# Performance work log

Measured on AMD Instinct MI355X. Metric: run time of the kernel, lower is better.

## Reference

```python
import jax, jax.numpy as jnp
import numpy as np
import math

B, N, T, D, H, NOUT = 32, 20, 100, 4, 128, 16
E = N * (N - 1)
EPS = 1e-5

def _conv1d(x, w, b):
    # x: [M, Cin, L], w: [Cout, Cin, K] -> [M, Cout, L-K+1] (VALID, stride 1)
    y = jax.lax.conv_general_dilated(x, w, (1,), 'VALID', dimension_numbers=('NCH', 'OIH', 'NCH'))
    return y + b[None, :, None]

def _bn(x, g, b, axes, caxis):
    # training-mode batch norm (biased variance), eps as in torch
    m = jnp.mean(x, axis=axes, keepdims=True)
    v = jnp.var(x, axis=axes, keepdims=True)
    sh = [1] * x.ndim
    sh[caxis] = -1
    return (x - m) / jnp.sqrt(v + EPS) * g.reshape(sh) + b.reshape(sh)

def _mlp(x, w1, b1, w2, b2, g, bb):
    h = jax.nn.elu(x @ w1.T + b1)
    h = jax.nn.elu(h @ w2.T + b2)
    return _bn(h, g, bb, (0, 1), 2)  # BN over B*E samples per feature

def _forward(rel_rec, rel_send, inputs, conv1_w, conv1_b, bn1_g, bn1_b, conv2_w, conv2_b, bn2_g, bn2_b, pred_w, pred_b, att_w, att_b, mlp1_w1, mlp1_b1, mlp1_w2, mlp1_b2, mlp1_g, mlp1_bb, mlp2_w1, mlp2_b1, mlp2_w2, mlp2_b2, mlp2_g, mlp2_bb, mlp3_w1, mlp3_b1, mlp3_w2, mlp3_b2, mlp3_g, mlp3_bb, fc_out_w, fc_out_b):
    Bv, Nv, Tv, Dv = inputs.shape
    Ev = Nv * (Nv - 1)
    # node2edge_temporal: gather sender/receiver trajectories -> [B*E, 2D, T]
    xf = inputs.reshape(Bv, Nv, Tv * Dv)
    recv = jnp.einsum('en,bnf->bef', rel_rec, xf).reshape(Bv * Ev, Tv, Dv).transpose(0, 2, 1)
    send = jnp.einsum('en,bnf->bef', rel_send, xf).reshape(Bv * Ev, Tv, Dv).transpose(0, 2, 1)
    edges = jnp.concatenate([send, recv], axis=1)
    # CNN over time
    h = jax.nn.relu(_conv1d(edges, conv1_w, conv1_b))
    h = _bn(h, bn1_g, bn1_b, (0, 2), 1)
    L = h.shape[-1] // 2
    h = h[:, :, : 2 * L].reshape(h.shape[0], h.shape[1], L, 2).max(axis=-1)  # maxpool k=2 s=2
    h = jax.nn.relu(_conv1d(h, conv2_w, conv2_b))
    h = _bn(h, bn2_g, bn2_b, (0, 2), 1)
    pred = jnp.einsum('bct,oc->bot', h, pred_w[:, :, 0]) + pred_b[None, :, None]
    att = jax.nn.softmax(jnp.einsum('bct,oc->bot', h, att_w[:, :, 0]) + att_b[None, :, None], axis=-1)
    x = (pred * att).mean(axis=-1).reshape(Bv, Ev, -1)  # attention-weighted mean pool
    x = _mlp(x, mlp1_w1, mlp1_b1, mlp1_w2, mlp1_b2, mlp1_g, mlp1_bb)
    x_skip = x
    # edge2node: scatter-mean into receivers (divide by N)
    xn = jnp.einsum('en,beh->bnh', rel_rec, x) / Nv
    xn = _mlp(xn, mlp2_w1, mlp2_b1, mlp2_w2, mlp2_b2, mlp2_g, mlp2_bb)
    # node2edge: gather back to edges
    es = jnp.einsum('en,bnh->beh', rel_send, xn)
    er = jnp.einsum('en,bnh->beh', rel_rec, xn)
    x = jnp.concatenate([es, er, x_skip], axis=2)
    x = _mlp(x, mlp3_w1, mlp3_b1, mlp3_w2, mlp3_b2, mlp3_g, mlp3_bb)
    return x @ fc_out_w.T + fc_out_b

def setup_inputs() -> dict:
    key = jax.random.key(0)
    ks = iter(jax.random.split(key, 64))
    def rn(shape, scale):
        return jax.random.normal(next(ks), shape, dtype=jnp.float32) * scale
    def xav(fo, fi):
        return rn((fo, fi), math.sqrt(2.0 / (fo + fi)))
    inputs = rn((B, N, T, D), 1.0)
    pairs = np.array([(i, j) for i in range(N) for j in range(N) if i != j])
    eye = np.eye(N, dtype=np.float32)
    d = {'inputs': inputs,
         'rel_rec': jnp.asarray(eye[pairs[:, 0]]),
         'rel_send': jnp.asarray(eye[pairs[:, 1]])}
    d['conv1_w'] = rn((H, 2 * D, 5), math.sqrt(2.0 / (5 * H)))
    d['conv1_b'] = jnp.full((H,), 0.1, jnp.float32)
    d['bn1_g'] = jnp.ones((H,), jnp.float32); d['bn1_b'] = jnp.zeros((H,), jnp.float32)
    d['conv2_w'] = rn((H, H, 5), math.sqrt(2.0 / (5 * H)))
    d['conv2_b'] = jnp.full((H,), 0.1, jnp.float32)
    d['bn2_g'] = jnp.ones((H,), jnp.float32); d['bn2_b'] = jnp.zeros((H,), jnp.float32)
    d['pred_w'] = rn((H, H, 1), math.sqrt(2.0 / H))
    d['pred_b'] = jnp.full((H,), 0.1, jnp.float32)
    d['att_w'] = rn((1, H, 1), math.sqrt(2.0))
    d['att_b'] = jnp.full((1,), 0.1, jnp.float32)
    for nm, fi in (('mlp1', H), ('mlp2', H), ('mlp3', 3 * H)):
        d[nm + '_w1'] = xav(H, fi); d[nm + '_b1'] = jnp.full((H,), 0.1, jnp.float32)
        d[nm + '_w2'] = xav(H, H); d[nm + '_b2'] = jnp.full((H,), 0.1, jnp.float32)
        d[nm + '_g'] = jnp.ones((H,), jnp.float32); d[nm + '_bb'] = jnp.zeros((H,), jnp.float32)
    d['fc_out_w'] = xav(NOUT, H)
    d['fc_out_b'] = jnp.full((NOUT,), 0.1, jnp.float32)
    return d

def reference(inputs, rel_rec, rel_send, conv1_w, conv1_b, bn1_g, bn1_b, conv2_w, conv2_b, bn2_g, bn2_b, pred_w, pred_b, att_w, att_b, mlp1_w1, mlp1_b1, mlp1_w2, mlp1_b2, mlp1_g, mlp1_bb, mlp2_w1, mlp2_b1, mlp2_w2, mlp2_b2, mlp2_g, mlp2_bb, mlp3_w1, mlp3_b1, mlp3_w2, mlp3_b2, mlp3_g, mlp3_bb, fc_out_w, fc_out_b):
    return _forward(rel_rec, rel_send, inputs, conv1_w, conv1_b, bn1_g, bn1_b, conv2_w, conv2_b, bn2_g, bn2_b, pred_w, pred_b, att_w, att_b, mlp1_w1, mlp1_b1, mlp1_w2, mlp1_b2, mlp1_g, mlp1_bb, mlp2_w1, mlp2_b1, mlp2_w2, mlp2_b2, mlp2_g, mlp2_bb, mlp3_w1, mlp3_b1, mlp3_w2, mlp3_b2, mlp3_g, mlp3_bb, fc_out_w, fc_out_b)
```

## Files before the change

kernel.cpp:

```cpp
#include <hip/hip_runtime.h>
#include <hip/hip_bf16.h>
#include <hip/hip_fp16.h>

#define BB 32
#define NN 20
#define TT 100
#define DD 4
#define HH 128
#define EE 380
#define BE 12160
#define L1 96
#define LP 48
#define L2 44
#define NOUT 16
#define EPS 1e-5f
#define NREP 64

typedef _Float16 f16x8 __attribute__((ext_vector_type(8)));
typedef _Float16 f16x4 __attribute__((ext_vector_type(4)));
typedef _Float16 f16x2 __attribute__((ext_vector_type(2)));
typedef float f32x4 __attribute__((ext_vector_type(4)));

#define S_BN1_SC 256
#define S_BN2_SC 768
#define S_M1_SC 1280
#define S_M2_SC 1792
#define S_M3_SC 2304

#define OFF_STATS 0ULL
#define OFF_SIDX 16384ULL
#define OFF_RIDX 18432ULL
#define OFF_INC 20480ULL
#define OFF_Y23 24576ULL
#define OFF_X 149446656ULL
#define OFF_BUFA 155672576ULL
#define OFF_BUFB 161898496ULL
#define OFF_XN 168124416ULL
#define OFF_T640 168452096ULL
#define OFF_REPM 168779776ULL
#define OFF_HF16 168845312ULL
#define OFF_MP 171958272ULL
#define OFF_APACK OFF_T640
#define OFF_APACK1 (OFF_T640 + 163840ULL)
#define OFF_PWT (OFF_T640 + 180224ULL)
#define OFF_REP1 OFF_BUFA
#define OFF_REP2 (OFF_BUFA + 65536ULL)
#define MP_M1W1 0
#define MP_M1W2 16384
#define MP_M2W1 32768
#define MP_M2W2 49152
#define MP_M3W2 65536
#define MP_M3W1 81920

__device__ __forceinline__ float eluf(float v) { return v > 0.f ? v : expm1f(v); }

__global__ __launch_bounds__(256) void k_prep(const float* __restrict__ rel_rec,
                                              const float* __restrict__ rel_send,
                                              const float* __restrict__ w2,
                                              const float* __restrict__ w1,
                                              const float* __restrict__ pred_w,
                                              const float* __restrict__ m1w1,
                                              const float* __restrict__ m1w2,
                                              const float* __restrict__ m2w1,
                                              const float* __restrict__ m2w2,
                                              const float* __restrict__ m3w1,
                                              const float* __restrict__ m3w2,
                                              _Float16* __restrict__ apack,
                                              _Float16* __restrict__ apack1,
                                              float* __restrict__ pwt,
                                              _Float16* __restrict__ mp,
                                              float* rep1, float* rep2, float* repm,
                                              int* sidx, int* ridx, int* inc) {
    int b = blockIdx.x;
    int tid = threadIdx.x;
    int l = tid & 63;
    if (b < 40) {
        int f = b * 4 + (tid >> 6);
        int m0 = f & 7, ks = f >> 3, s = ks & 3, k = ks >> 2;
        int m = m0 * 16 + (l & 15);
        int cbase = 32 * s + (l >> 4) * 8;
#pragma unroll
        for (int j = 0; j < 8; ++j)
            apack[(f * 64 + l) * 8 + j] = (_Float16)w2[m * 640 + (cbase + j) * 5 + k];
    } else if (b < 44) {
        int f = (b - 40) * 4 + (tid >> 6);
        int m0 = f & 7, s = f >> 3;
        int m = m0 * 16 + (l & 15);
        int cbase = 32 * s + (l >> 4) * 8;
#pragma unroll
        for (int j = 0; j < 8; ++j) {
            int c = cbase + j;
            apack1[(f * 64 + l) * 8 + j] = (c < 40) ? (_Float16)w1[m * 40 + c] : (_Float16)0.f;
        }
    } else if (b == 44) {
        for (int i = tid; i < NREP * 256; i += 256) { rep1[i] = 0.f; rep2[i] = 0.f; repm[i] = 0.f; }
        for (int e = tid; e < EE; e += 256) {
            int s = 0, r = 0;
            for (int n = 0; n < NN; ++n) {
                if (rel_send[e * NN + n] > 0.5f) s = n;
                if (rel_rec[e * NN + n] > 0.5f) r = n;
            }
            sidx[e] = s; ridx[e] = r;
        }
        __syncthreads();
        if (tid < NN) {
            int k = 0;
            for (int e = 0; e < EE; ++e)
                if (ridx[e] == tid) inc[tid * (NN - 1) + (k++)] = e;
        }
    } else if (b < 53) {
        int idx = (b - 45) * 2048 + tid;
        for (int rep = 0; rep < 8; ++rep, idx += 256) {
            int o = idx >> 7, c = idx & 127;
            pwt[c * 128 + o] = pred_w[idx];
        }
    } else {
        int idx = b - 53;
        const float* W; _Float16* dst; int K;
        if (idx < 8)       { W = m1w1; dst = mp + MP_M1W1; K = 128; }
        else if (idx < 16) { W = m1w2; dst = mp + MP_M1W2; K = 128; idx -= 8; }
        else if (idx < 24) { W = m2w1; dst = mp + MP_M2W1; K = 128; idx -= 16; }
        else if (idx < 32) { W = m2w2; dst = mp + MP_M2W2; K = 128; idx -= 24; }
        else if (idx < 40) { W = m3w2; dst = mp + MP_M3W2; K = 128; idx -= 32; }
        else               { W = m3w1; dst = mp + MP_M3W1; K = 384; idx -= 40; }
        int f = idx * 4 + (tid >> 6);
        int s = f >> 3, m0 = f & 7;
        int m = m0 * 16 + (l & 15);
        int cb = 32 * s + (l >> 4) * 8;
#pragma unroll
        for (int j = 0; j < 8; ++j)
            dst[(f * 64 + l) * 8 + j] = (_Float16)W[m * K + cb + j];
    }
}

__device__ __forceinline__ void load_edges(float* s_edges,
                                           const float* __restrict__ inputs,
                                           int b, int sn, int rn) {
    for (int i = threadIdx.x; i < 800; i += 256) {
        int ci = i / 100, t = i - ci * 100;
        int n = (ci < 4) ? sn : rn;
        int d = ci & 3;
        s_edges[ci * 100 + t] = inputs[((b * NN + n) * TT + t) * DD + d];
    }
}

__device__ __forceinline__ void build_x1(_Float16* s_x1, const float* s_edges) {
    for (int i = threadIdx.x; i < 96 * 64; i += 256) {
        int t = i >> 6, c = i & 63;
        float v = 0.f;
        if (c < 40) {
            int ci = (c * 205) >> 10;
            int k = c - 5 * ci;
            v = s_edges[ci * 100 + t + k];
        }
        s_x1[t * 72 + c] = (_Float16)v;
    }
}

__device__ __forceinline__ void conv1_mfma(const _Float16* __restrict__ apack1,
                                           const _Float16* s_x1,
                                           int w, int lane, int quad, int l15,
                                           f32x4 acc1[2][6]) {
#pragma unroll
    for (int m = 0; m < 2; ++m)
#pragma unroll
        for (int nt = 0; nt < 6; ++nt) acc1[m][nt] = (f32x4){0.f, 0.f, 0.f, 0.f};
    const f16x8* Ap = (const f16x8*)apack1;
#pragma unroll
    for (int s = 0; s < 2; ++s) {
        f16x8 a0 = Ap[(s * 8 + 2 * w) * 64 + lane];
        f16x8 a1 = Ap[(s * 8 + 2 * w + 1) * 64 + lane];
#pragma unroll
        for (int nt = 0; nt < 6; ++nt) {
            f16x8 bfr = *(const f16x8*)((const char*)s_x1 +
                                        (nt * 16 + l15) * 144 + 64 * s + quad * 16);
            acc1[0][nt] = __builtin_amdgcn_mfma_f32_16x16x32_f16(a0, bfr, acc1[0][nt], 0, 0, 0);
            acc1[1][nt] = __builtin_amdgcn_mfma_f32_16x16x32_f16(a1, bfr, acc1[1][nt], 0, 0, 0);
        }
    }
}

__global__ __launch_bounds__(256) void k_conv1_stats(const float* __restrict__ inputs,
                                                     const _Float16* __restrict__ apack1,
                                                     const float* __restrict__ conv1_b,
                                                     const int* __restrict__ sidx,
                                                     const int* __restrict__ ridx,
                                                     float* rep1,
                                                     _Float16* __restrict__ y2p) {
    __shared__ float s_edges[800];
    __shared__ __align__(16) _Float16 s_x1[96 * 72];
    __shared__ __align__(16) _Float16 s_y2t[48 * 136];
    int be = blockIdx.x;
    int b = be / EE, e = be - b * EE;
    float* rep = rep1 + (be & (NREP - 1)) * 256;
    load_edges(s_edges, inputs, b, sidx[e], ridx[e]);
    __syncthreads();
    build_x1(s_x1, s_edges);
    __syncthreads();
    int w = threadIdx.x >> 6, lane = threadIdx.x & 63;
    int quad = lane >> 4, l15 = lane & 15;
    f32x4 acc1[2][6];
    conv1_mfma(apack1, s_x1, w, lane, quad, l15, acc1);
#pragma unroll
    for (int m = 0; m < 2; ++m) {
        int co0 = (2 * w + m) * 16 + quad * 4;
        float ss[4] = {0.f, 0.f, 0.f, 0.f}, qq[4] = {0.f, 0.f, 0.f, 0.f};
#pragma unroll
        for (int nt = 0; nt < 6; ++nt) {
            int t = nt * 16 + l15;
#pragma unroll
            for (int r = 0; r < 4; ++r) {
                float v = fmaxf(acc1[m][nt][r] + conv1_b[co0 + r], 0.f);
                ss[r] += v; qq[r] += v * v;
                float p = __shfl_xor(v, 1);
                if ((l15 & 1) == 0)
                    s_y2t[(t >> 1) * 136 + co0 + r] = (_Float16)fmaxf(v, p);
            }
        }
#pragma unroll
        for (int r = 0; r < 4; ++r) {
            float s = ss[r], q = qq[r];
            s += __shfl_xor(s, 1); s += __shfl_xor(s, 2); s += __shfl_xor(s, 4); s += __shfl_xor(s, 8);
            q += __shfl_xor(q, 1); q += __shfl_xor(q, 2); q += __shfl_xor(q, 4); q += __shfl_xor(q, 8);
            if (l15 == 0) {
                atomicAdd(&rep[co0 + r], s);
                atomicAdd(&rep[128 + co0 + r], q);
            }
        }
    }
    __syncthreads();
    _Float16* dst = y2p + (long long)be * 6144;
    for (int chunk = threadIdx.x; chunk < 768; chunk += 256) {
        int row = chunk >> 4, off = (chunk & 15) * 8;
        *(f16x8*)(dst + row * 128 + off) = *(const f16x8*)(&s_y2t[row * 136 + off]);
    }
}

__global__ void k_finalize_rep(float* __restrict__ rep, float* stats, int scIdx,
                               const float* __restrict__ g, const float* __restrict__ bb,
                               float inv_count) {
    int j = threadIdx.x;
    float s = 0.f, q = 0.f;
    for (int i = 0; i < NREP; ++i) {
        s += rep[i * 256 + j];
        q += rep[i * 256 + 128 + j];
    }
    for (int i = 0; i < NREP; ++i) {
        rep[i * 256 + j] = 0.f;
        rep[i * 256 + 128 + j] = 0.f;
    }
    float m = s * inv_count;
    float v = fmaxf(q * inv_count - m * m, 0.f);
    float sc = g[j] * rsqrtf(v + EPS);
    stats[scIdx + j] = sc;
    stats[scIdx + 128 + j] = bb[j] - m * sc;
}

__global__ __launch_bounds__(256) void k_conv2(_Float16* __restrict__ y23,
                                               const _Float16* __restrict__ apack,
                                               const float* __restrict__ conv2_b,
                                               const float* __restrict__ stats,
                                               float* rep2) {
    __shared__ __align__(16) _Float16 s_y2t[2][52 * 136];
    int tid = threadIdx.x;
    int be0 = blockIdx.x * 2;
    for (int i = tid; i < 544; i += 256) {
        int ed = i / 272, rem = i - ed * 272;
        ((int*)(&s_y2t[ed][48 * 136]))[rem] = 0;
    }
    {
        int c0 = (tid & 15) * 8;
        float4 sca = *(const float4*)(stats + S_BN1_SC + c0);
        float4 scb = *(const float4*)(stats + S_BN1_SC + c0 + 4);
        float4 sha = *(const float4*)(stats + S_BN1_SC + 128 + c0);
        float4 shb = *(const float4*)(stats + S_BN1_SC + 128 + c0 + 4);
        for (int i = tid; i < 1536; i += 256) {
            int ed = i / 768, rem = i - ed * 768;
            int row = rem >> 4;
            f16x8 g = *(const f16x8*)(y23 + (long long)(be0 + ed) * 6144 + row * 128 + c0);
            f16x8 o;
            o[0] = (_Float16)fmaf((float)g[0], sca.x, sha.x);
            o[1] = (_Float16)fmaf((float)g[1], sca.y, sha.y);
            o[2] = (_Float16)fmaf((float)g[2], sca.z, sha.z);
            o[3] = (_Float16)fmaf((float)g[3], sca.w, sha.w);
            o[4] = (_Float16)fmaf((float)g[4], scb.x, shb.x);
            o[5] = (_Float16)fmaf((float)g[5], scb.y, shb.y);
            o[6] = (_Float16)fmaf((float)g[6], scb.z, shb.z);
            o[7] = (_Float16)fmaf((float)g[7], scb.w, shb.w);
            *(f16x8*)(&s_y2t[ed][row * 136 + c0]) = o;
        }
    }
    __syncthreads();
    int w = tid >> 6, lane = tid & 63;
    int quad = lane >> 4, l15 = lane & 15;
    int g = w & 1, e = w >> 1;
    f32x4 acc[4][3];
#pragma unroll
    for (int m = 0; m < 4; ++m)
#pragma unroll
        for (int nt = 0; nt < 3; ++nt) acc[m][nt] = (f32x4){0.f, 0.f, 0.f, 0.f};
    const f16x8* Ap = (const f16x8*)apack;
    const char* base = (const char*)&s_y2t[e][0];
#pragma unroll
    for (int k = 0; k < 5; ++k) {
#pragma unroll
        for (int s = 0; s < 4; ++s) {
            f16x8 am[4];
#pragma unroll
            for (int m = 0; m < 4; ++m)
                am[m] = Ap[((k * 4 + s) * 8 + g * 4 + m) * 64 + lane];
#pragma unroll
            for (int nt = 0; nt < 3; ++nt) {
                f16x8 bfr = *(const f16x8*)(base + (nt * 16 + l15 + k) * 272 + 64 * s + quad * 16);
#pragma unroll
                for (int m = 0; m < 4; ++m)
                    acc[m][nt] = __builtin_amdgcn_mfma_f32_16x16x32_f16(am[m], bfr, acc[m][nt], 0, 0, 0);
            }
        }
    }
    int be = be0 + e;
    _Float16* y3 = y23 + (long long)be * 6144;
    float* rep = rep2 + (be & (NREP - 1)) * 256;
#pragma unroll
    for (int m = 0; m < 4; ++m) {
        int co0 = (g * 4 + m) * 16 + quad * 4;
        float ssum[4] = {0.f, 0.f, 0.f, 0.f}, qsum[4] = {0.f, 0.f, 0.f, 0.f};
#pragma unroll
        for (int nt = 0; nt < 3; ++nt) {
            int t = nt * 16 + l15;
            bool valid = t < 44;
#pragma unroll
            for (int r = 0; r < 4; ++r) {
                float v = fmaxf(acc[m][nt][r] + conv2_b[co0 + r], 0.f);
                if (valid) {
                    y3[(co0 + r) * 44 + t] = (_Float16)v;
                    ssum[r] += v; qsum[r] += v * v;
                }
            }
        }
#pragma unroll
        for (int r = 0; r < 4; ++r) {
            float s = ssum[r], q = qsum[r];
            s += __shfl_xor(s, 1); s += __shfl_xor(s, 2); s += __shfl_xor(s, 4); s += __shfl_xor(s, 8);
            q += __shfl_xor(q, 1); q += __shfl_xor(q, 2); q += __shfl_xor(q, 4); q += __shfl_xor(q, 8);
            if (l15 == 0) {
                atomicAdd(&rep[co0 + r], s);
                atomicAdd(&rep[128 + co0 + r], q);
            }
        }
    }
}

__global__ __launch_bounds__(256) void k_predatt(const _Float16* __restrict__ y23,
                                                 const float* __restrict__ stats,
                                                 const float* __restrict__ att_w,
                                                 const float* __restrict__ att_b,
                                                 const float* __restrict__ pwt,
                                                 const float* __restrict__ pred_b,
                                                 float* __restrict__ x) {
    __shared__ float h[128 * 45];
    __shared__ float s_att[48];
    __shared__ float s_p1[256];
    __shared__ float s_p2[256];
    __shared__ float s_sc[128], s_sh[128];
    int be = blockIdx.x, tid = threadIdx.x;
    if (tid < 128) {
        s_sc[tid] = stats[S_BN2_SC + tid];
        s_sh[tid] = stats[S_BN2_SC + 128 + tid];
    }
    __syncthreads();
    const f16x2* yp = (const f16x2*)(y23 + (long long)be * 6144);
    for (int i = tid; i < 2816; i += 256) {
        int c = i / 22, t2 = i - c * 22;
        f16x2 v = yp[i];
        float sc = s_sc[c], sh = s_sh[c];
        h[c * 45 + 2 * t2] = fmaf((float)v[0], sc, sh);
        h[c * 45 + 2 * t2 + 1] = fmaf((float)v[1], sc, sh);
    }
    __syncthreads();
    int w = tid >> 6, lane = tid & 63;
    {
        float aw0 = att_w[lane], aw1 = att_w[64 + lane];
        for (int tt = 0; tt < 11; ++tt) {
            int t = w * 11 + tt;
            float p = h[lane * 45 + t] * aw0 + h[(64 + lane) * 45 + t] * aw1;
            p += __shfl_xor(p, 1); p += __shfl_xor(p, 2); p += __shfl_xor(p, 4);
            p += __shfl_xor(p, 8); p += __shfl_xor(p, 16); p += __shfl_xor(p, 32);
            if (lane == 0) s_att[t] = p + att_b[0];
        }
    }
    __syncthreads();
    if (w == 0) {
        float v = (lane < 44) ? s_att[lane] : -1e30f;
        float m = v;
        m = fmaxf(m, __shfl_xor(m, 1)); m = fmaxf(m, __shfl_xor(m, 2));
        m = fmaxf(m, __shfl_xor(m, 4)); m = fmaxf(m, __shfl_xor(m, 8));
        m = fmaxf(m, __shfl_xor(m, 16)); m = fmaxf(m, __shfl_xor(m, 32));
        float ev = (lane < 44) ? expf(v - m) : 0.f;
        float ss = ev;
        ss += __shfl_xor(ss, 1); ss += __shfl_xor(ss, 2); ss += __shfl_xor(ss, 4);
        ss += __shfl_xor(ss, 8); ss += __shfl_xor(ss, 16); ss += __shfl_xor(ss, 32);
        if (lane < 44) s_att[lane] = ev / ss;
    }
    __syncthreads();
    {
        int c = tid & 127, hh = tid >> 7;
        float a = 0.f;
        for (int t = hh * 22; t < hh * 22 + 22; ++t) a = fmaf(h[c * 45 + t], s_att[t], a);
        s_p1[tid] = a;
    }
    __syncthreads();
    {
        int o = tid & 127, hh = tid >> 7;
        float a = 0.f;
        for (int c = hh * 64; c < hh * 64 + 64; ++c) {
            float hw = s_p1[c] + s_p1[128 + c];
            a = fmaf(pwt[c * 128 + o], hw, a);
        }
        s_p2[tid] = a;
    }
    __syncthreads();
    if (tid < 128) {
        float a = s_p2[tid] + s_p2[128 + tid] + pred_b[tid];
        x[(long long)be * 128 + tid] = a * (1.0f / 44.0f);
    }
}

template <bool IN16, bool OUT16, bool STATS>
__global__ __launch_bounds__(256) void k_linmm(const void* __restrict__ inV,
                                               const _Float16* __restrict__ wp,
                                               const float* __restrict__ bias,
                                               void* __restrict__ outV,
                                               float* __restrict__ repm) {
    __shared__ __align__(16) _Float16 s_b[64 * 136];
    int tid = threadIdx.x;
    long long r0 = (long long)blockIdx.x * 64;
    if (IN16) {
        const f16x8* src = (const f16x8*)((const _Float16*)inV + r0 * 128);
        for (int i = tid; i < 1024; i += 256) {
            int row = i >> 4, c0 = (i & 15) * 8;
            *(f16x8*)(&s_b[row * 136 + c0]) = src[i];
        }
    } else {
        const float4* src = (const float4*)((const float*)inV + r0 * 128);
        for (int i = tid; i < 2048; i += 256) {
            int row = i >> 5, c0 = (i & 31) * 4;
            float4 v = src[i];
            f16x4 o = {(_Float16)v.x, (_Float16)v.y, (_Float16)v.z, (_Float16)v.w};
            *(f16x4*)(&s_b[row * 136 + c0]) = o;
        }
    }
    __syncthreads();
    int w = tid >> 6, lane = tid & 63, quad = lane >> 4, l15 = lane & 15;
    f32x4 acc[2][4];
#pragma unroll
    for (int m = 0; m < 2; ++m)
#pragma unroll
        for (int nt = 0; nt < 4; ++nt) acc[m][nt] = (f32x4){0.f, 0.f, 0.f, 0.f};
    const f16x8* Ap = (const f16x8*)wp;
#pragma unroll
    for (int s = 0; s < 4; ++s) {
        f16x8 a0 = Ap[(s * 8 + 2 * w) * 64 + lane];
        f16x8 a1 = Ap[(s * 8 + 2 * w + 1) * 64 + lane];
#pragma unroll
        for (int nt = 0; nt < 4; ++nt) {
            f16x8 bfr = *(const f16x8*)((const char*)s_b + (nt * 16 + l15) * 272 + 64 * s + quad * 16);
            acc[0][nt] = __builtin_amdgcn_mfma_f32_16x16x32_f16(a0, bfr, acc[0][nt], 0, 0, 0);
            acc[1][nt] = __builtin_amdgcn_mfma_f32_16x16x32_f16(a1, bfr, acc[1][nt], 0, 0, 0);
        }
    }
#pragma unroll
    for (int m = 0; m < 2; ++m) {
        int j0 = (2 * w + m) * 16 + quad * 4;
        float4 bs = *(const float4*)(bias + j0);
        float ss[4] = {0.f, 0.f, 0.f, 0.f}, qq[4] = {0.f, 0.f, 0.f, 0.f};
#pragma unroll
        for (int nt = 0; nt < 4; ++nt) {
            int row = nt * 16 + l15;
            float v0 = eluf(acc[m][nt][0] + bs.x);
            float v1 = eluf(acc[m][nt][1] + bs.y);
            float v2 = eluf(acc[m][nt][2] + bs.z);
            float v3 = eluf(acc[m][nt][3] + bs.w);
            if (OUT16) {
                f16x4 o = {(_Float16)v0, (_Float16)v1, (_Float16)v2, (_Float16)v3};
                *(f16x4*)((_Float16*)outV + (r0 + row) * 128 + j0) = o;
            } else {
                float4 o = {v0, v1, v2, v3};
                *(float4*)((float*)outV + (r0 + row) * 128 + j0) = o;
            }
            if (STATS) {
                ss[0] += v0; qq[0] += v0 * v0;
                ss[1] += v1; qq[1] += v1 * v1;
                ss[2] += v2; qq[2] += v2 * v2;
                ss[3] += v3; qq[3] += v3 * v3;
            }
        }
        if (STATS) {
            float* rep = repm + (blockIdx.x & (NREP - 1)) * 256;
#pragma unroll
            for (int r = 0; r < 4; ++r) {
                float s = ss[r], q = qq[r];
                s += __shfl_xor(s, 1); s += __shfl_xor(s, 2); s += __shfl_xor(s, 4); s += __shfl_xor(s, 8);
                q += __shfl_xor(q, 1); q += __shfl_xor(q, 2); q += __shfl_xor(q, 4); q += __shfl_xor(q, 8);
                if (l15 == 0) {
                    atomicAdd(&rep[j0 + r], s);
                    atomicAdd(&rep[128 + j0 + r], q);
                }
            }
        }
    }
}

__global__ __launch_bounds__(256) void k_linmm3(const float* __restrict__ xn,
                                                const float* __restrict__ bufB,
                                                const int* __restrict__ sidx,
                                                const int* __restrict__ ridx,
                                                const float* __restrict__ stats,
                                                const _Float16* __restrict__ wp,
                                                const float* __restrict__ bias,
                                                _Float16* __restrict__ out) {
    __shared__ __align__(16) _Float16 s_b[64 * 392];
    __shared__ float s_st[4][128];
    __shared__ int s_s[64], s_r[64];
    int tid = threadIdx.x;
    long long r0 = (long long)blockIdx.x * 64;
    if (tid < 128) {
        s_st[0][tid] = stats[S_M2_SC + tid];
        s_st[1][tid] = stats[S_M2_SC + 128 + tid];
        s_st[2][tid] = stats[S_M1_SC + tid];
        s_st[3][tid] = stats[S_M1_SC + 128 + tid];
    }
    if (tid < 64) {
        int r = (int)r0 + tid, b = r / EE, ed = r - b * EE;
        s_s[tid] = (b * NN + sidx[ed]) * 128;
        s_r[tid] = (b * NN + ridx[ed]) * 128;
    }
    __syncthreads();
    for (int i = tid; i < 8192; i += 256) {
        int row = i >> 7, j = i & 127;
        float sc2 = s_st[0][j], sh2 = s_st[1][j];
        s_b[row * 392 + j] = (_Float16)fmaf(xn[s_s[row] + j], sc2, sh2);
        s_b[row * 392 + 128 + j] = (_Float16)fmaf(xn[s_r[row] + j], sc2, sh2);
        s_b[row * 392 + 256 + j] = (_Float16)fmaf(bufB[(r0 + row) * 128 + j], s_st[2][j], s_st[3][j]);
    }
    __syncthreads();
    int w = tid >> 6, lane = tid & 63, quad = lane >> 4, l15 = lane & 15;
    f32x4 acc[2][4];
#pragma unroll
    for (int m = 0; m < 2; ++m)
#pragma unroll
        for (int nt = 0; nt < 4; ++nt) acc[m][nt] = (f32x4){0.f, 0.f, 0.f, 0.f};
    const f16x8* Ap = (const f16x8*)wp;
#pragma unroll
    for (int s = 0; s < 12; ++s) {
        f16x8 a0 = Ap[(s * 8 + 2 * w) * 64 + lane];
        f16x8 a1 = Ap[(s * 8 + 2 * w + 1) * 64 + lane];
#pragma unroll
        for (int nt = 0; nt < 4; ++nt) {
            f16x8 bfr = *(const f16x8*)((const char*)s_b + (nt * 16 + l15) * 784 + 64 * s + quad * 16);
            acc[0][nt] = __builtin_amdgcn_mfma_f32_16x16x32_f16(a0, bfr, acc[0][nt], 0, 0, 0);
            acc[1][nt] = __builtin_amdgcn_mfma_f32_16x16x32_f16(a1, bfr, acc[1][nt], 0, 0, 0);
        }
    }
#pragma unroll
    for (int m = 0; m < 2; ++m) {
        int j0 = (2 * w + m) * 16 + quad * 4;
        float4 bs = *(const float4*)(bias + j0);
#pragma unroll
        for (int nt = 0; nt < 4; ++nt) {
            int row = nt * 16 + l15;
            f16x4 o = {(_Float16)eluf(acc[m][nt][0] + bs.x),
                       (_Float16)eluf(acc[m][nt][1] + bs.y),
                       (_Float16)eluf(acc[m][nt][2] + bs.z),
                       (_Float16)eluf(acc[m][nt][3] + bs.w)};
            *(f16x4*)(out + (r0 + row) * 128 + j0) = o;
        }
    }
}

__global__ __launch_bounds__(128) void k_e2n(const float* __restrict__ bufB,
                                             const int* __restrict__ inc,
                                             const float* __restrict__ stats,
                                             float* __restrict__ xn) {
    int bn = blockIdx.x;
    int b = bn / NN, n = bn - b * NN;
    int j = threadIdx.x;
    float sc = stats[S_M1_SC + j], sh = stats[S_M1_SC + 128 + j];
    float s = 0.f;
    for (int k = 0; k < NN - 1; ++k) {
        int e = inc[n * (NN - 1) + k];
        s += bufB[(long long)(b * EE + e) * 128 + j];
    }
    xn[bn * 128 + j] = (s * sc + (float)(NN - 1) * sh) * (1.0f / (float)NN);
}

__global__ __launch_bounds__(256) void k_fcout(const float* __restrict__ h2,
                                               const float* __restrict__ stats,
                                               const float* __restrict__ fcw,
                                               const float* __restrict__ fcb,
                                               float* __restrict__ out) {
    __shared__ float s_x[16 * 129];
    __shared__ float s_w[16 * 129];
    int r0 = blockIdx.x * 16;
    int tid = threadIdx.x;
    for (int i = tid; i < 16 * 128; i += 256) {
        int rr = i >> 7, j = i & 127;
        s_x[rr * 129 + j] = fmaf(h2[(long long)(r0 + rr) * 128 + j],
                                 stats[S_M3_SC + j], stats[S_M3_SC + 128 + j]);
    }
    for (int i = tid; i < 16 * 128; i += 256) {
        int o = i >> 7, j = i & 127;
        s_w[o * 129 + j] = fcw[i];
    }
    __syncthreads();
    int rl = tid >> 4, o = tid & 15;
    float a = fcb[o];
    for (int j = 0; j < 128; ++j) a = fmaf(s_x[rl * 129 + j], s_w[o * 129 + j], a);
    out[(long long)(r0 + rl) * 16 + o] = a;
}

extern "C" void kernel_launch(void* const* d_in, const int* in_sizes, int n_in,
                              void* d_out, int out_size, void* d_ws, size_t ws_size,
                              hipStream_t stream) {
    const float* inputs = (const float*)d_in[0];
    const float* rel_rec = (const float*)d_in[1];
    const float* rel_send = (const float*)d_in[2];
    const float* conv1_w = (const float*)d_in[3];
    const float* conv1_b = (const float*)d_in[4];
    const float* bn1_g = (const float*)d_in[5];
    const float* bn1_b = (const float*)d_in[6];
    const float* conv2_w = (const float*)d_in[7];
    const float* conv2_b = (const float*)d_in[8];
    const float* bn2_g = (const float*)d_in[9];
    const float* bn2_b = (const float*)d_in[10];
    const float* pred_w = (const float*)d_in[11];
    const float* pred_b = (const float*)d_in[12];
    const float* att_w = (const float*)d_in[13];
    const float* att_b = (const float*)d_in[14];
    const float* m1w1 = (const float*)d_in[15];
    const float* m1b1 = (const float*)d_in[16];
    const float* m1w2 = (const float*)d_in[17];
    const float* m1b2 = (const float*)d_in[18];
    const float* m1g = (const float*)d_in[19];
    const float* m1bb = (const float*)d_in[20];
    const float* m2w1 = (const float*)d_in[21];
    const float* m2b1 = (const float*)d_in[22];
    const float* m2w2 = (const float*)d_in[23];
    const float* m2b2 = (const float*)d_in[24];
    const float* m2g = (const float*)d_in[25];
    const float* m2bb = (const float*)d_in[26];
    const float* m3w1 = (const float*)d_in[27];
    const float* m3b1 = (const float*)d_in[28];
    const float* m3w2 = (const float*)d_in[29];
    const float* m3b2 = (const float*)d_in[30];
    const float* m3g = (const float*)d_in[31];
    const float* m3bb = (const float*)d_in[32];
    const float* fcw = (const float*)d_in[33];
    const float* fcb = (const float*)d_in[34];

    char* ws = (char*)d_ws;
    float* stats = (float*)(ws + OFF_STATS);
    int* sidx = (int*)(ws + OFF_SIDX);
    int* ridx = (int*)(ws + OFF_RIDX);
    int* inc = (int*)(ws + OFF_INC);
    _Float16* y23 = (_Float16*)(ws + OFF_Y23);
    float* x = (float*)(ws + OFF_X);
    float* bufB = (float*)(ws + OFF_BUFB);
    float* xn = (float*)(ws + OFF_XN);
    _Float16* apack = (_Float16*)(ws + OFF_APACK);
    _Float16* apack1 = (_Float16*)(ws + OFF_APACK1);
    float* pwt = (float*)(ws + OFF_PWT);
    float* rep1 = (float*)(ws + OFF_REP1);
    float* rep2 = (float*)(ws + OFF_REP2);
    float* repm = (float*)(ws + OFF_REPM);
    _Float16* hf16 = (_Float16*)(ws + OFF_HF16);
    _Float16* mp = (_Float16*)(ws + OFF_MP);
    float* outp = (float*)d_out;

    hipLaunchKernelGGL(k_prep, dim3(117), dim3(256), 0, stream,
                       rel_rec, rel_send, conv2_w, conv1_w, pred_w,
                       m1w1, m1w2, m2w1, m2w2, m3w1, m3w2,
                       apack, apack1, pwt, mp, rep1, rep2, repm, sidx, ridx, inc);
    hipLaunchKernelGGL(k_conv1_stats, dim3(BE), dim3(256), 0, stream,
                       inputs, apack1, conv1_b, sidx, ridx, rep1, y23);
    hipLaunchKernelGGL(k_finalize_rep, dim3(1), dim3(128), 0, stream,
                       rep1, stats, S_BN1_SC, bn1_g, bn1_b, 1.0f / (float)(BE * L1));
    hipLaunchKernelGGL(k_conv2, dim3(BE / 2), dim3(256), 0, stream,
                       y23, apack, conv2_b, stats, rep2);
    hipLaunchKernelGGL(k_finalize_rep, dim3(1), dim3(128), 0, stream,
                       rep2, stats, S_BN2_SC, bn2_g, bn2_b, 1.0f / (float)(BE * L2));
    hipLaunchKernelGGL(k_predatt, dim3(BE), dim3(256), 0, stream,
                       y23, stats, att_w, att_b, pwt, pred_b, x);
    hipLaunchKernelGGL((k_linmm<false, true, false>), dim3(BE / 64), dim3(256), 0, stream,
                       (const void*)x, mp + MP_M1W1, m1b1, (void*)hf16, repm);
    hipLaunchKernelGGL((k_linmm<true, false, true>), dim3(BE / 64), dim3(256), 0, stream,
                       (const void*)hf16, mp + MP_M1W2, m1b2, (void*)bufB, repm);
    hipLaunchKernelGGL(k_finalize_rep, dim3(1), dim3(128), 0, stream,
                       repm, stats, S_M1_SC, m1g, m1bb, 1.0f / (float)BE);
    hipLaunchKernelGGL(k_e2n, dim3(BB * NN), dim3(128), 0, stream, bufB, inc, stats, xn);
    hipLaunchKernelGGL((k_linmm<false, true, false>), dim3(BB * NN / 64), dim3(256), 0, stream,
                       (const void*)xn, mp + MP_M2W1, m2b1, (void*)hf16, repm);
    hipLaunchKernelGGL((k_linmm<true, false, true>), dim3(BB * NN / 64), dim3(256), 0, stream,
                       (const void*)hf16, mp + MP_M2W2, m2b2, (void*)xn, repm);
    hipLaunchKernelGGL(k_finalize_rep, dim3(1), dim3(128), 0, stream,
                       repm, stats, S_M2_SC, m2g, m2bb, 1.0f / (float)(BB * NN));
    hipLaunchKernelGGL(k_linmm3, dim3(BE / 64), dim3(256), 0, stream,
                       xn, bufB, sidx, ridx, stats, mp + MP_M3W1, m3b1, hf16);
    hipLaunchKernelGGL((k_linmm<true, false, true>), dim3(BE / 64), dim3(256), 0, stream,
                       (const void*)hf16, mp + MP_M3W2, m3b2, (void*)bufB, repm);
    hipLaunchKernelGGL(k_finalize_rep, dim3(1), dim3(128), 0, stream,
                       repm, stats, S_M3_SC, m3g, m3bb, 1.0f / (float)BE);
    hipLaunchKernelGGL(k_fcout, dim3(BE / 16), dim3(256), 0, stream, bufB, stats, fcw, fcb, outp);
    (void)in_sizes; (void)n_in; (void)out_size; (void)ws_size;
}
```

Baseline: 633.9 us.

## Read conv1 B operand directly from transposed edge tile, drop im2col buffer

```diff
diff --git a/kernel.cpp b/kernel.cpp
--- a/kernel.cpp
+++ b/kernel.cpp
@@ -90,7 +90,9 @@
 #pragma unroll
         for (int j = 0; j < 8; ++j) {
             int c = cbase + j;
-            apack1[(f * 64 + l) * 8 + j] = (c < 40) ? (_Float16)w1[m * 40 + c] : (_Float16)0.f;
+            int k = c >> 3, ci = c & 7;
+            apack1[(f * 64 + l) * 8 + j] = (k < 5) ? (_Float16)w1[m * 40 + ci * 5 + k]
+                                                   : (_Float16)0.f;
         }
     } else if (b == 44) {
         for (int i = tid; i < NREP * 256; i += 256) { rep1[i] = 0.f; rep2[i] = 0.f; repm[i] = 0.f; }
@@ -133,53 +135,6 @@
     }
 }
 
-__device__ __forceinline__ void load_edges(float* s_edges,
-                                           const float* __restrict__ inputs,
-                                           int b, int sn, int rn) {
-    for (int i = threadIdx.x; i < 800; i += 256) {
-        int ci = i / 100, t = i - ci * 100;
-        int n = (ci < 4) ? sn : rn;
-        int d = ci & 3;
-        s_edges[ci * 100 + t] = inputs[((b * NN + n) * TT + t) * DD + d];
-    }
-}
-
-__device__ __forceinline__ void build_x1(_Float16* s_x1, const float* s_edges) {
-    for (int i = threadIdx.x; i < 96 * 64; i += 256) {
-        int t = i >> 6, c = i & 63;
-        float v = 0.f;
-        if (c < 40) {
-            int ci = (c * 205) >> 10;
-            int k = c - 5 * ci;
-            v = s_edges[ci * 100 + t + k];
-        }
-        s_x1[t * 72 + c] = (_Float16)v;
-    }
-}
-
-__device__ __forceinline__ void conv1_mfma(const _Float16* __restrict__ apack1,
-                                           const _Float16* s_x1,
-                                           int w, int lane, int quad, int l15,
-                                           f32x4 acc1[2][6]) {
-#pragma unroll
-    for (int m = 0; m < 2; ++m)
-#pragma unroll
-        for (int nt = 0; nt < 6; ++nt) acc1[m][nt] = (f32x4){0.f, 0.f, 0.f, 0.f};
-    const f16x8* Ap = (const f16x8*)apack1;
-#pragma unroll
-    for (int s = 0; s < 2; ++s) {
-        f16x8 a0 = Ap[(s * 8 + 2 * w) * 64 + lane];
-        f16x8 a1 = Ap[(s * 8 + 2 * w + 1) * 64 + lane];
-#pragma unroll
-        for (int nt = 0; nt < 6; ++nt) {
-            f16x8 bfr = *(const f16x8*)((const char*)s_x1 +
-                                        (nt * 16 + l15) * 144 + 64 * s + quad * 16);
-            acc1[0][nt] = __builtin_amdgcn_mfma_f32_16x16x32_f16(a0, bfr, acc1[0][nt], 0, 0, 0);
-            acc1[1][nt] = __builtin_amdgcn_mfma_f32_16x16x32_f16(a1, bfr, acc1[1][nt], 0, 0, 0);
-        }
-    }
-}
-
 __global__ __launch_bounds__(256) void k_conv1_stats(const float* __restrict__ inputs,
                                                      const _Float16* __restrict__ apack1,
                                                      const float* __restrict__ conv1_b,
@@ -187,20 +142,43 @@
                                                      const int* __restrict__ ridx,
                                                      float* rep1,
                                                      _Float16* __restrict__ y2p) {
-    __shared__ float s_edges[800];
-    __shared__ __align__(16) _Float16 s_x1[96 * 72];
+    __shared__ __align__(16) _Float16 s_edgesT[104 * 8];
     __shared__ __align__(16) _Float16 s_y2t[48 * 136];
     int be = blockIdx.x;
     int b = be / EE, e = be - b * EE;
+    int sn = sidx[e], rn = ridx[e];
     float* rep = rep1 + (be & (NREP - 1)) * 256;
-    load_edges(s_edges, inputs, b, sidx[e], ridx[e]);
-    __syncthreads();
-    build_x1(s_x1, s_edges);
+    for (int i = threadIdx.x; i < 200; i += 256) {
+        int side = (i >= 100) ? 1 : 0;
+        int t = i - side * 100;
+        int n = side ? rn : sn;
+        float4 v = *(const float4*)(inputs + ((long long)(b * NN + n) * TT + t) * DD);
+        f16x4 o = {(_Float16)v.x, (_Float16)v.y, (_Float16)v.z, (_Float16)v.w};
+        *(f16x4*)(&s_edgesT[t * 8 + side * 4]) = o;
+    }
+    if (threadIdx.x < 32) s_edgesT[800 + threadIdx.x] = (_Float16)0.f;
     __syncthreads();
     int w = threadIdx.x >> 6, lane = threadIdx.x & 63;
     int quad = lane >> 4, l15 = lane & 15;
     f32x4 acc1[2][6];
-    conv1_mfma(apack1, s_x1, w, lane, quad, l15, acc1);
+#pragma unroll
+    for (int m = 0; m < 2; ++m)
+#pragma unroll
+        for (int nt = 0; nt < 6; ++nt) acc1[m][nt] = (f32x4){0.f, 0.f, 0.f, 0.f};
+    {
+        const f16x8* Ap = (const f16x8*)apack1;
+#pragma unroll
+        for (int s = 0; s < 2; ++s) {
+            f16x8 a0 = Ap[(s * 8 + 2 * w) * 64 + lane];
+            f16x8 a1 = Ap[(s * 8 + 2 * w + 1) * 64 + lane];
+#pragma unroll
+            for (int nt = 0; nt < 6; ++nt) {
+                f16x8 bfr = *(const f16x8*)(&s_edgesT[(nt * 16 + l15 + 4 * s + quad) * 8]);
+                acc1[0][nt] = __builtin_amdgcn_mfma_f32_16x16x32_f16(a0, bfr, acc1[0][nt], 0, 0, 0);
+                acc1[1][nt] = __builtin_amdgcn_mfma_f32_16x16x32_f16(a1, bfr, acc1[1][nt], 0, 0, 0);
+            }
+        }
+    }
 #pragma unroll
     for (int m = 0; m < 2; ++m) {
         int co0 = (2 * w + m) * 16 + quad * 4;
```

Result: faster. 597.1 us (-5.8%).
